# Optimization experiments

Measured on AMD Instinct MI355X. Metric: run time of the kernel, lower is better.

Reference implementation:

```python
import jax, jax.numpy as jnp
import numpy as np

SEQ = 4096
STATE_DIM = 512
ACTION_DIM = 496
T_DIM = 16
EMBED = STATE_DIM + ACTION_DIM + T_DIM  # 1024
HEADS = 4
HEAD_DIM = EMBED // HEADS
FF = 4096
N_EXP = 8
TOP_K = 2
EPS = 1e-5


def _ln(x, g, b):
    m = jnp.mean(x, -1, keepdims=True)
    v = jnp.var(x, -1, keepdims=True)
    return (x - m) * jax.lax.rsqrt(v + EPS) * g + b


def setup_inputs() -> dict:
    key = jax.random.key(0)
    ks = jax.random.split(key, 24)
    s = lambda k, shape, scale=0.02: jax.random.normal(k, shape, dtype=jnp.float32) * scale
    return {
        "x": jax.random.normal(ks[0], (SEQ, ACTION_DIM), dtype=jnp.float32),
        "time": jax.random.randint(ks[1], (SEQ,), 0, 6),
        "state": jax.random.normal(ks[2], (SEQ, 1, STATE_DIM), dtype=jnp.float32),
        "time_table": s(ks[3], (6, T_DIM), 1.0),
        "expert_w": s(ks[4], (N_EXP, EMBED, EMBED)),   # [n, in, out]
        "expert_b": jnp.zeros((N_EXP, EMBED), jnp.float32),
        "gate_w": s(ks[5], (EMBED, N_EXP)),
        "gate_b": jnp.zeros((N_EXP,), jnp.float32),
        "in_proj_w": s(ks[6], (EMBED, 3 * EMBED)),
        "in_proj_b": jnp.zeros((3 * EMBED,), jnp.float32),
        "out_proj_w": s(ks[7], (EMBED, EMBED)),
        "out_proj_b": jnp.zeros((EMBED,), jnp.float32),
        "ln1_g": jnp.ones((EMBED,), jnp.float32),
        "ln1_b": jnp.zeros((EMBED,), jnp.float32),
        "ff1_w": s(ks[8], (EMBED, FF)),
        "ff1_b": jnp.zeros((FF,), jnp.float32),
        "ff2_w": s(ks[9], (FF, ACTION_DIM)),
        "ff2_b": jnp.zeros((ACTION_DIM,), jnp.float32),
        "ln2_g": jnp.ones((ACTION_DIM,), jnp.float32),
        "ln2_b": jnp.zeros((ACTION_DIM,), jnp.float32),
    }


def reference(x, time, state, time_table, expert_w, expert_b, gate_w, gate_b,
              in_proj_w, in_proj_b, out_proj_w, out_proj_b,
              ln1_g, ln1_b, ff1_w, ff1_b, ff2_w, ff2_b, ln2_g, ln2_b):
    # combine inputs -> [S, EMBED]
    t_emb = time_table[time]                      # [S, t_dim]
    h = jnp.concatenate([x, t_emb, state[:, 0, :]], axis=-1)

    # MoE: softmax gate, top-k combine over densely-computed expert outputs
    gate = jax.nn.softmax(h @ gate_w + gate_b, axis=-1)      # [S, N]
    scores, idx = jax.lax.top_k(gate, TOP_K)                 # [S, K]
    all_out = jnp.einsum('se,nef->snf', h, expert_w) + expert_b[None]  # [S, N, E]
    comb = jnp.zeros_like(gate).at[jnp.arange(SEQ)[:, None], idx].add(scores)
    moe = jnp.einsum('sn,snf->sf', comb, all_out)            # [S, E]

    # multi-head self-attention (torch nn.MultiheadAttention, unbatched)
    qkv = moe @ in_proj_w + in_proj_b
    q, k, v = jnp.split(qkv, 3, axis=-1)
    q = q.reshape(SEQ, HEADS, HEAD_DIM) * (HEAD_DIM ** -0.5)
    k = k.reshape(SEQ, HEADS, HEAD_DIM)
    v = v.reshape(SEQ, HEADS, HEAD_DIM)
    att = jax.nn.softmax(jnp.einsum('shd,thd->hst', q, k), axis=-1)
    ao = jnp.einsum('hst,thd->shd', att, v).reshape(SEQ, EMBED)
    ao = ao @ out_proj_w + out_proj_b

    out1 = _ln(moe + ao, ln1_g, ln1_b)
    ff = jax.nn.relu(out1 @ ff1_w + ff1_b) @ ff2_w + ff2_b   # [S, action_dim]
    return _ln(ff, ln2_g, ln2_b)
```

## Files before the change

### kernel.cpp

```cpp
#include <hip/hip_runtime.h>
#include <hip/hip_bf16.h>
#include <hip/hip_fp8.h>

typedef __hip_bfloat16 hb;
typedef __bf16 bf16x8 __attribute__((ext_vector_type(8)));
typedef __bf16 bf16x4 __attribute__((ext_vector_type(4)));
typedef float f32x4 __attribute__((ext_vector_type(4)));

#define SEQ 4096
#define EMBED 1024
#define NHEAD 4
#define HDIM 256
#define FFD 4096
#define NEXP 8
#define ADIM 496
#define NSLOT 9216

static __device__ __forceinline__ float b2f(hb x) { return __bfloat162float(x); }
static __device__ __forceinline__ hb f2b(float x) { return __float2bfloat16(x); }
static __device__ __forceinline__ unsigned char f2e4m3(float v) {
  __hip_fp8_e4m3 t(v);
  return t.__x;
}
static __device__ __forceinline__ unsigned char f2e4m3_fast(float x) {
  unsigned u = __float_as_uint(x);
  u += 0x7FFFFu + ((u >> 20) & 1u);
  return (unsigned char)((u >> 20) - 960u);
}

#define GLOAD_LDS16(g, l)                                                      \
  __builtin_amdgcn_global_load_lds(                                            \
      (const __attribute__((address_space(1))) void*)(g),                      \
      (__attribute__((address_space(3))) void*)(l), 16, 0, 0)

#define GEMM_KLOOP64(KMAX)                                                     \
  for (int kt = 0; kt < (KMAX); kt += 64) {                                    \
    GLOAD_LDS16(Ag + kt, sA + wave * 512);                                     \
    GLOAD_LDS16(Ag + kt + 32, sA + 4096 + wave * 512);                         \
    GLOAD_LDS16(Ag + kt + 64 * lda_, sA + 2048 + wave * 512);                  \
    GLOAD_LDS16(Ag + kt + 64 * lda_ + 32, sA + 6144 + wave * 512);             \
    GLOAD_LDS16(Bg + kt, sB + wave * 512);                                     \
    GLOAD_LDS16(Bg + kt + 32, sB + 4096 + wave * 512);                         \
    GLOAD_LDS16(Bg + kt + 64 * ldb_, sB + 2048 + wave * 512);                  \
    GLOAD_LDS16(Bg + kt + 64 * ldb_ + 32, sB + 6144 + wave * 512);             \
    __syncthreads();                                                           \
    _Pragma("unroll") for (int ks = 0; ks < 2; ks++) {                         \
      bf16x8 av[4], bv[4];                                                     \
      _Pragma("unroll") for (int i = 0; i < 4; i++) {                          \
        const int row = wr * 64 + i * 16 + lm;                                 \
        av[i] = *(const bf16x8*)&sA[ks * 4096 + row * 32 + sw8];               \
      }                                                                        \
      _Pragma("unroll") for (int i = 0; i < 4; i++) {                          \
        const int row = wc * 64 + i * 16 + lm;                                 \
        bv[i] = *(const bf16x8*)&sB[ks * 4096 + row * 32 + sw8];               \
      }                                                                        \
      _Pragma("unroll") for (int i = 0; i < 4; i++)                            \
          _Pragma("unroll") for (int j = 0; j < 4; j++) acc[i][j] =            \
          __builtin_amdgcn_mfma_f32_16x16x32_bf16(av[i], bv[j], acc[i][j], 0,  \
                                                  0, 0);                       \
    }                                                                          \
    __syncthreads();                                                           \
  }

#define GEMM_PROLOGUE                                                          \
  const int m0 = blockIdx.y * 128, n0 = blockIdx.x * 128;                      \
  const int tid = threadIdx.x;                                                 \
  const int wave = tid >> 6, lane = tid & 63;                                  \
  const int quad = lane >> 4, lm = lane & 15;                                  \
  const int wr = wave >> 1, wc = wave & 1;                                     \
  const int r0 = tid >> 2;                                                     \
  const int cg = 8 * ((tid & 3) ^ ((tid >> 2) & 3));                           \
  const int sw8 = (quad ^ (lm & 3)) * 8;

#define EPILOGUE_B16(DST, LDC)                                                 \
  {                                                                            \
    hb* eb = smem + wave * 1024;                                               \
    _Pragma("unroll") for (int i = 0; i < 4; i++) {                            \
      _Pragma("unroll") for (int j = 0; j < 4; j++) {                          \
        const int c = ((j ^ quad) << 4) + lm;                                  \
        _Pragma("unroll") for (int rr = 0; rr < 4; rr++)                       \
            eb[(quad * 4 + rr) * 64 + c] = f2b(acc[i][j][rr]);                 \
      }                                                                        \
      _Pragma("unroll") for (int p = 0; p < 2; p++) {                          \
        const int r = p * 8 + (lane >> 3);                                     \
        const int cgc = lane & 7;                                              \
        const int gs = (cgc >> 1) ^ (r >> 2);                                  \
        const bf16x8 val =                                                     \
            *(const bf16x8*)&eb[r * 64 + gs * 16 + (cgc & 1) * 8];             \
        const long grow = m0 + wr * 64 + i * 16 + r;                           \
        *(bf16x8*)&DST[grow * (LDC) + n0 + wc * 64 + cgc * 8] = val;           \
      }                                                                        \
    }                                                                          \
  }

__global__ __launch_bounds__(256) void gemm_bt(
    const hb* __restrict__ A, long lda, long bA,
    const hb* __restrict__ B, long ldb, long bB,
    hb* __restrict__ C, long ldc, long bC,
    int K, const float* __restrict__ bias, int relu) {
  __shared__ __align__(16) hb smem[2 * 128 * 64];
  hb* sA = smem;
  hb* sB = smem + 8192;
  const int z = blockIdx.z;
  A += (long)z * bA;
  B += (long)z * bB;
  C += (long)z * bC;
  GEMM_PROLOGUE
  const long lda_ = lda, ldb_ = ldb;
  const hb* Ag = A + (long)(m0 + r0) * lda + cg;
  const hb* Bg = B + (long)(n0 + r0) * ldb + cg;

  f32x4 acc[4][4] = {};
  GEMM_KLOOP64(K)

  hb* eb = smem + wave * 1024;
#pragma unroll
  for (int i = 0; i < 4; i++) {
#pragma unroll
    for (int j = 0; j < 4; j++) {
      const float bval = bias ? bias[n0 + wc * 64 + j * 16 + lm] : 0.f;
      const int c = ((j ^ quad) << 4) + lm;
#pragma unroll
      for (int rr = 0; rr < 4; rr++) {
        float v = acc[i][j][rr] + bval;
        if (relu) v = fmaxf(v, 0.f);
        eb[(quad * 4 + rr) * 64 + c] = f2b(v);
      }
    }
#pragma unroll
    for (int p = 0; p < 2; p++) {
      const int r = p * 8 + (lane >> 3);
      const int cgc = lane & 7;
      const int gs = (cgc >> 1) ^ (r >> 2);
      const bf16x8 val = *(const bf16x8*)&eb[r * 64 + gs * 16 + (cgc & 1) * 8];
      const long grow = m0 + wr * 64 + i * 16 + r;
      *(bf16x8*)&C[grow * ldc + n0 + wc * 64 + cgc * 8] = val;
    }
  }
}

__global__ __launch_bounds__(256) void gemm_bt_exp(
    const hb* __restrict__ A, long lda, long bA,
    const hb* __restrict__ B, long ldb, long bB,
    unsigned char* __restrict__ C, long ldc, long bC,
    int K, float scale, hb* __restrict__ rsP) {
  __shared__ __align__(16) hb smem[2 * 128 * 64];
  hb* sA = smem;
  hb* sB = smem + 8192;
  const int z = blockIdx.z;
  A += (long)z * bA;
  B += (long)z * bB;
  C += (long)z * bC;
  GEMM_PROLOGUE
  const long lda_ = lda, ldb_ = ldb;
  const hb* Ag = A + (long)(m0 + r0) * lda + cg;
  const hb* Bg = B + (long)(n0 + r0) * ldb + cg;

  f32x4 acc[4][4] = {};
  GEMM_KLOOP64(K)

  unsigned char* eb8 = (unsigned char*)smem + wave * 1024;
  float* rbuf = (float*)sB;
  float rs[4][4];
#pragma unroll
  for (int i = 0; i < 4; i++) {
    float r4[4] = {0.f, 0.f, 0.f, 0.f};
#pragma unroll
    for (int j = 0; j < 4; j++) {
      const int c = ((j ^ quad) << 4) + lm;
#pragma unroll
      for (int rr = 0; rr < 4; rr++) {
        const float e =
            fminf(fmaxf(__expf(acc[i][j][rr] * scale), 0.015625f), 448.f);
        r4[rr] += e;
        eb8[(quad * 4 + rr) * 64 + c] = f2e4m3_fast(e);
      }
    }
#pragma unroll
    for (int rr = 0; rr < 4; rr++) {
      r4[rr] += __shfl_xor(r4[rr], 1);
      r4[rr] += __shfl_xor(r4[rr], 2);
      r4[rr] += __shfl_xor(r4[rr], 4);
      r4[rr] += __shfl_xor(r4[rr], 8);
      rs[i][rr] = r4[rr];
    }
    {
      const int r = lane >> 2;
      const int cgc = lane & 3;
      const f32x4 val =
          *(const f32x4*)&eb8[r * 64 + ((cgc ^ (r >> 2)) << 4)];
      const long grow = m0 + wr * 64 + i * 16 + r;
      *(f32x4*)&C[grow * ldc + n0 + wc * 64 + cgc * 16] = val;
    }
  }
  if (lm == 0) {
#pragma unroll
    for (int i = 0; i < 4; i++)
#pragma unroll
      for (int rr = 0; rr < 4; rr++)
        rbuf[(wr * 2 + wc) * 64 + i * 16 + quad * 4 + rr] = rs[i][rr];
  }
  __syncthreads();
  if (tid < 128) {
    const int lwr = tid >> 6, r64 = tid & 63;
    const float d = rbuf[lwr * 128 + r64] + rbuf[lwr * 128 + 64 + r64];
    rsP[((long)blockIdx.x * gridDim.z + z) * SEQ + m0 + lwr * 64 + r64] =
        f2b(d);
  }
}

__global__ __launch_bounds__(256) void pv_f8_splitk(
    const unsigned char* __restrict__ S, const unsigned char* __restrict__ Vt,
    hb* __restrict__ Cp) {
  const int z = blockIdx.z;
  const int head = z >> 1, split = z & 1;
  const unsigned char* A = S + (long)head * SEQ * SEQ + split * 2048;
  const unsigned char* B = Vt + ((long)head << 20) + split * 2048;
  hb* Cb = Cp + (long)z * SEQ * 256;
  __shared__ __align__(16) unsigned char smem8[16384];
  hb* smem = (hb*)smem8;
  unsigned char* sA8 = smem8;
  unsigned char* sB8 = smem8 + 8192;
  const int m0 = blockIdx.y * 128, n0 = blockIdx.x * 128;
  const int tid = threadIdx.x;
  const int wave = tid >> 6, lane = tid & 63;
  const int quad = lane >> 4, lm = lane & 15;
  const int wr = wave >> 1, wc = wave & 1;
  const int r8 = tid >> 2;
  const int cg8 = 16 * ((tid & 3) ^ (r8 & 3));
  const unsigned char* Ag = A + (long)(m0 + r8) * 4096 + cg8;
  const unsigned char* Bg = B + (long)(n0 + r8) * 4096 + cg8;

  f32x4 acc[4][4] = {};
  for (int kt = 0; kt < 2048; kt += 64) {
    GLOAD_LDS16(Ag + kt, sA8 + wave * 1024);
    GLOAD_LDS16(Ag + kt + 64 * 4096, sA8 + 4096 + wave * 1024);
    GLOAD_LDS16(Bg + kt, sB8 + wave * 1024);
    GLOAD_LDS16(Bg + kt + 64 * 4096, sB8 + 4096 + wave * 1024);
    __syncthreads();
#pragma unroll
    for (int ks = 0; ks < 2; ks++) {
      long a8[4], b8[4];
#pragma unroll
      for (int i = 0; i < 4; i++) {
        const int row = wr * 64 + i * 16 + lm;
        a8[i] = *(const long*)&sA8[row * 64 +
                                   (((ks * 2 + (quad >> 1)) ^ (row & 3)) << 4) +
                                   (quad & 1) * 8];
      }
#pragma unroll
      for (int i = 0; i < 4; i++) {
        const int row = wc * 64 + i * 16 + lm;
        b8[i] = *(const long*)&sB8[row * 64 +
                                   (((ks * 2 + (quad >> 1)) ^ (row & 3)) << 4) +
                                   (quad & 1) * 8];
      }
#pragma unroll
      for (int i = 0; i < 4; i++)
#pragma unroll
        for (int j = 0; j < 4; j++)
          acc[i][j] = __builtin_amdgcn_mfma_f32_16x16x32_fp8_fp8(
              a8[i], b8[j], acc[i][j], 0, 0, 0);
    }
    __syncthreads();
  }
  EPILOGUE_B16(Cb, 256)
}

__global__ __launch_bounds__(256) void gemm_bt_splitk(
    const hb* __restrict__ A, long lda, long bA,
    const hb* __restrict__ B, long ldb, long bB,
    float* __restrict__ Cp, int ldcp, long pstride, int Ksub, int shift) {
  const int z = blockIdx.z;
  const int batch = z >> shift, split = z - (batch << shift);
  A += (long)batch * bA + (long)split * Ksub;
  B += (long)batch * bB + (long)split * Ksub;
  Cp += (long)z * pstride;
  __shared__ __align__(16) hb smem[2 * 128 * 64];
  hb* sA = smem;
  hb* sB = smem + 8192;
  GEMM_PROLOGUE
  const long lda_ = lda, ldb_ = ldb;
  const hb* Ag = A + (long)(m0 + r0) * lda + cg;
  const hb* Bg = B + (long)(n0 + r0) * ldb + cg;

  f32x4 acc[4][4] = {};
  GEMM_KLOOP64(Ksub)

  float* ef = (float*)smem + wave * 1024;
#pragma unroll
  for (int i = 0; i < 4; i++) {
#pragma unroll
    for (int j = 0; j < 4; j++) {
      const int c = ((j ^ quad) << 4) + lm;
#pragma unroll
      for (int rr = 0; rr < 4; rr++)
        ef[(quad * 4 + rr) * 64 + c] = acc[i][j][rr];
    }
#pragma unroll
    for (int p = 0; p < 4; p++) {
      const int r = p * 4 + (lane >> 4);
      const int cgc = lane & 15;
      const int gs = (cgc >> 2) ^ (r >> 2);
      const f32x4 val = *(const f32x4*)&ef[r * 64 + gs * 16 + (cgc & 3) * 4];
      const long grow = m0 + wr * 64 + i * 16 + r;
      *(f32x4*)&Cp[grow * ldcp + n0 + wc * 64 + cgc * 4] = val;
    }
  }
}

__global__ __launch_bounds__(256) void gemm_bt_splitk_b16(
    const hb* __restrict__ A, long lda, long bA,
    const hb* __restrict__ B, long ldb, long bB,
    hb* __restrict__ Cp, int ldcp, long pstride, int Ksub, int shift) {
  const int z = blockIdx.z;
  const int batch = z >> shift, split = z - (batch << shift);
  A += (long)batch * bA + (long)split * Ksub;
  B += (long)batch * bB + (long)split * Ksub;
  Cp += (long)z * pstride;
  __shared__ __align__(16) hb smem[2 * 128 * 64];
  hb* sA = smem;
  hb* sB = smem + 8192;
  GEMM_PROLOGUE
  const long lda_ = lda, ldb_ = ldb;
  const hb* Ag = A + (long)(m0 + r0) * lda + cg;
  const hb* Bg = B + (long)(n0 + r0) * ldb + cg;

  f32x4 acc[4][4] = {};
  GEMM_KLOOP64(Ksub)
  EPILOGUE_B16(Cp, ldcp)
}

__global__ __launch_bounds__(256) void reduce_splitk(
    const float* __restrict__ part, long pstride, int nsplit, int shift,
    hb* __restrict__ C, long ldc, long bC, int Nshift) {
  const long idx = (long)blockIdx.x * 256 + threadIdx.x;
  const int batch = blockIdx.y;
  float v = 0.f;
  for (int k = 0; k < nsplit; k++)
    v += part[(long)((batch << shift) + k) * pstride + idx];
  const long row = idx >> Nshift;
  const long col = idx & ((1 << Nshift) - 1);
  C[(long)batch * bC + row * ldc + col] = f2b(v);
}

__global__ __launch_bounds__(256) void reduce_pv(
    const hb* __restrict__ part, const hb* __restrict__ rsP,
    hb* __restrict__ ao) {
  const int rb = blockIdx.x * 4, head = blockIdx.y, tid = threadIdx.x;
  __shared__ float dsh[4];
  if (tid < 128) {
    const int r = tid >> 5, nb = tid & 31;
    float p = b2f(rsP[((long)nb * NHEAD + head) * SEQ + rb + r]);
#pragma unroll
    for (int o = 16; o; o >>= 1) p += __shfl_down(p, o, 32);
    if (nb == 0) dsh[r] = p;
  }
  __syncthreads();
  const int r = tid >> 6, c4 = (tid & 63) * 4;
  const float den = dsh[r];
  const long base = ((long)(head * 2) * SEQ + rb + r) * 256 + c4;
  const bf16x4 p0 = *(const bf16x4*)&part[base];
  const bf16x4 p1 = *(const bf16x4*)&part[base + (long)SEQ * 256];
  bf16x4 o4;
#pragma unroll
  for (int k = 0; k < 4; k++)
    o4[k] = (__bf16)(((float)p0[k] + (float)p1[k]) / den);
  *(bf16x4*)&ao[(long)(rb + r) * 1024 + head * 256 + c4] = o4;
}

__global__ __launch_bounds__(256) void gemm_moe(
    const hb* __restrict__ h, const hb* __restrict__ expertT,
    const int* __restrict__ slot_token, const int* __restrict__ eblk,
    hb* __restrict__ slotout) {
  const int e = eblk[blockIdx.y];
  if (e < 0) return;
  __shared__ __align__(16) hb smem[2 * 128 * 64];
  hb* sA = smem;
  hb* sB = smem + 8192;
  GEMM_PROLOGUE
  const int t0 = slot_token[m0 + r0];
  const int t1 = slot_token[m0 + r0 + 64];
  const hb* B = expertT + ((long)e << 20);
  const hb* Ag0 = h + (long)t0 * EMBED + cg;
  const hb* Ag1 = h + (long)t1 * EMBED + cg;
  const hb* Bg = B + (long)(n0 + r0) * EMBED + cg;

  f32x4 acc[4][4] = {};
  for (int kt = 0; kt < EMBED; kt += 64) {
    GLOAD_LDS16(Ag0 + kt, sA + wave * 512);
    GLOAD_LDS16(Ag0 + kt + 32, sA + 4096 + wave * 512);
    GLOAD_LDS16(Ag1 + kt, sA + 2048 + wave * 512);
    GLOAD_LDS16(Ag1 + kt + 32, sA + 6144 + wave * 512);
    GLOAD_LDS16(Bg + kt, sB + wave * 512);
    GLOAD_LDS16(Bg + kt + 32, sB + 4096 + wave * 512);
    GLOAD_LDS16(Bg + kt + 64 * EMBED, sB + 2048 + wave * 512);
    GLOAD_LDS16(Bg + kt + 64 * EMBED + 32, sB + 6144 + wave * 512);
    __syncthreads();
#pragma unroll
    for (int ks = 0; ks < 2; ks++) {
      bf16x8 av[4], bv[4];
#pragma unroll
      for (int i = 0; i < 4; i++) {
        const int row = wr * 64 + i * 16 + lm;
        av[i] = *(const bf16x8*)&sA[ks * 4096 + row * 32 + sw8];
      }
#pragma unroll
      for (int i = 0; i < 4; i++) {
        const int row = wc * 64 + i * 16 + lm;
        bv[i] = *(const bf16x8*)&sB[ks * 4096 + row * 32 + sw8];
      }
#pragma unroll
      for (int i = 0; i < 4; i++)
#pragma unroll
        for (int j = 0; j < 4; j++)
          acc[i][j] = __builtin_amdgcn_mfma_f32_16x16x32_bf16(av[i], bv[j],
                                                              acc[i][j], 0, 0, 0);
    }
    __syncthreads();
  }
  EPILOGUE_B16(slotout, EMBED)
}

__global__ __launch_bounds__(256) void transpose_all(
    const float* __restrict__ expert_w, const float* __restrict__ in_proj_w,
    const float* __restrict__ out_proj_w, const float* __restrict__ ff1_w,
    const float* __restrict__ ff2_w, hb* __restrict__ expertT,
    hb* __restrict__ inprojT, hb* __restrict__ outprojT, hb* __restrict__ ff1T,
    hb* __restrict__ ff2T) {
  const int b = blockIdx.x;
  const float* in;
  hb* outp;
  int Cin, ldin, ldout, bx, by;
  if (b < 4096) {
    const int z = b >> 9, l = b & 511;
    bx = l & 31; by = l >> 5;
    in = expert_w + (long)z * 1048576; outp = expertT + (long)z * 1048576;
    Cin = 1024; ldin = 1024; ldout = 1024;
  } else if (b < 5632) {
    const int l = b - 4096;
    bx = l % 96; by = l / 96;
    in = in_proj_w; outp = inprojT;
    Cin = 3072; ldin = 3072; ldout = 1024;
  } else if (b < 6144) {
    const int l = b - 5632;
    bx = l & 31; by = l >> 5;
    in = out_proj_w; outp = outprojT;
    Cin = 1024; ldin = 1024; ldout = 1024;
  } else if (b < 8192) {
    const int l = b - 6144;
    bx = l & 127; by = l >> 7;
    in = ff1_w; outp = ff1T;
    Cin = 4096; ldin = 4096; ldout = 1024;
  } else {
    const int l = b - 8192;
    bx = l & 15; by = l >> 4;
    in = ff2_w; outp = ff2T;
    Cin = 496; ldin = 496; ldout = 4096;
  }
  __shared__ hb tile[32][72];
  const int c0 = bx * 32, r0 = by * 64;
  const int t = threadIdx.x;
  {
    const int rr = t >> 2, cb = (t & 3) * 8;
    const int c = c0 + cb;
    float v[8] = {0, 0, 0, 0, 0, 0, 0, 0};
    if (c < Cin) {
      const f32x4 p0 = *(const f32x4*)&in[(long)(r0 + rr) * ldin + c];
      const f32x4 p1 = *(const f32x4*)&in[(long)(r0 + rr) * ldin + c + 4];
#pragma unroll
      for (int k = 0; k < 4; k++) { v[k] = p0[k]; v[4 + k] = p1[k]; }
    }
#pragma unroll
    for (int j = 0; j < 8; j++) {
      const int cidx = cb + j;
      tile[cidx][rr ^ ((((cidx) >> 3) & 3) << 3)] = f2b(v[j]);
    }
  }
  __syncthreads();
  {
    const int oc = t >> 3, seg = t & 7;
    const bf16x8 val = *(const bf16x8*)&tile[oc][(seg ^ ((oc >> 3) & 3)) * 8];
    *(bf16x8*)&outp[(long)(c0 + oc) * ldout + r0 + seg * 8] = val;
  }
}

__global__ __launch_bounds__(256) void transpose_v(
    const hb* __restrict__ in, hb* __restrict__ out) {
  __shared__ hb tile[32][33];
  const int z = blockIdx.z;
  in += (long)z * 256;
  out += (long)z * 1048576;
  const int c0 = blockIdx.x * 32, r0 = blockIdx.y * 32;
  const int tx = threadIdx.x, ty = threadIdx.y;
#pragma unroll
  for (int i = 0; i < 32; i += 8)
    tile[ty + i][tx] = in[(long)(r0 + ty + i) * 3072 + c0 + tx];
  __syncthreads();
#pragma unroll
  for (int i = 0; i < 32; i += 8)
    out[(long)(c0 + ty + i) * 4096 + r0 + tx] = tile[tx][ty + i];
}

__global__ __launch_bounds__(256) void transpose_v8(
    const hb* __restrict__ in, unsigned char* __restrict__ out) {
  __shared__ hb tile[32][33];
  const int z = blockIdx.z;
  in += (long)z * 256;
  out += (long)z * 1048576;
  const int c0 = blockIdx.x * 32, r0 = blockIdx.y * 32;
  const int tx = threadIdx.x, ty = threadIdx.y;
#pragma unroll
  for (int i = 0; i < 32; i += 8)
    tile[ty + i][tx] = in[(long)(r0 + ty + i) * 3072 + c0 + tx];
  __syncthreads();
#pragma unroll
  for (int i = 0; i < 32; i += 8)
    out[(long)(c0 + ty + i) * 4096 + r0 + tx] = f2e4m3(b2f(tile[tx][ty + i]));
}

__global__ __launch_bounds__(256) void bh_gate_kernel(
    const float* __restrict__ x, const int* __restrict__ timev,
    const float* __restrict__ state, const float* __restrict__ ttab,
    const float* __restrict__ gw, const float* __restrict__ gb,
    hb* __restrict__ h, int* __restrict__ tok_e, float* __restrict__ tok_w) {
  const int s = blockIdx.x, tid = threadIdx.x;
  const int wv = tid >> 6, ln = tid & 63;
  const int t = timev[s];
  const int c = tid * 4;
  f32x4 v4;
  if (c < ADIM)
    v4 = *(const f32x4*)&x[(long)s * ADIM + c];
  else if (c < 512)
    v4 = *(const f32x4*)&ttab[t * 16 + (c - ADIM)];
  else
    v4 = *(const f32x4*)&state[(long)s * 512 + (c - 512)];
  bf16x4 h4;
#pragma unroll
  for (int k = 0; k < 4; k++) h4[k] = (__bf16)v4[k];
  *(bf16x4*)&h[(long)s * EMBED + c] = h4;
  float acc[8] = {0, 0, 0, 0, 0, 0, 0, 0};
#pragma unroll
  for (int k = 0; k < 4; k++) {
    const float* g = gw + (c + k) * 8;
#pragma unroll
    for (int n = 0; n < 8; n++) acc[n] += v4[k] * g[n];
  }
#pragma unroll
  for (int o = 32; o; o >>= 1)
#pragma unroll
    for (int n = 0; n < 8; n++) acc[n] += __shfl_down(acc[n], o);
  __shared__ float red[4][8];
  if (ln == 0)
#pragma unroll
    for (int n = 0; n < 8; n++) red[wv][n] = acc[n];
  __syncthreads();
  if (tid == 0) {
    float lg[8], m = -1e30f;
    for (int n = 0; n < 8; n++) {
      lg[n] = red[0][n] + red[1][n] + red[2][n] + red[3][n] + gb[n];
      m = fmaxf(m, lg[n]);
    }
    float den = 0.f;
    for (int n = 0; n < 8; n++) {
      lg[n] = expf(lg[n] - m);
      den += lg[n];
    }
    for (int n = 0; n < 8; n++) lg[n] /= den;
    int i1 = 0;
    for (int n = 1; n < 8; n++)
      if (lg[n] > lg[i1]) i1 = n;
    int i2 = (i1 == 0) ? 1 : 0;
    for (int n = 0; n < 8; n++) {
      if (n == i1) continue;
      if (lg[n] > lg[i2]) i2 = n;
    }
    tok_e[2 * s] = i1;
    tok_w[2 * s] = lg[i1];
    tok_e[2 * s + 1] = i2;
    tok_w[2 * s + 1] = lg[i2];
  }
}

__global__ __launch_bounds__(256) void group_kernel(
    const int* __restrict__ tok_e, int* __restrict__ slot_token,
    int* __restrict__ token_slot, int* __restrict__ eblk) {
  __shared__ int cnt[8], off[9], cur[8];
  const int tid = threadIdx.x;
  if (tid < 8) cnt[tid] = 0;
  for (int i = tid; i < NSLOT; i += 256) slot_token[i] = 0;
  __syncthreads();
  for (int i = tid; i < 2 * SEQ; i += 256) atomicAdd(&cnt[tok_e[i]], 1);
  __syncthreads();
  if (tid == 0) {
    int o = 0;
    for (int n = 0; n < 8; n++) {
      off[n] = o;
      cur[n] = o;
      o += (cnt[n] + 127) & ~127;
    }
    off[8] = o;
  }
  __syncthreads();
  if (tid < NSLOT / 128) {
    const int rb = tid * 128;
    int e = -1;
    for (int n = 0; n < 8; n++)
      if (rb >= off[n] && rb < off[n + 1]) e = n;
    eblk[tid] = e;
  }
  for (int i = tid; i < 2 * SEQ; i += 256) {
    const int e = tok_e[i];
    const int slot = atomicAdd(&cur[e], 1);
    slot_token[slot] = i >> 1;
    token_slot[i] = slot;
  }
}

__global__ __launch_bounds__(256) void moe_combine_kernel(
    const hb* __restrict__ slotout, const int* __restrict__ token_slot,
    const float* __restrict__ tok_w, const int* __restrict__ tok_e,
    const float* __restrict__ eb, hb* __restrict__ moe) {
  const int s = blockIdx.x, tid = threadIdx.x;
  const int s0 = token_slot[2 * s], s1 = token_slot[2 * s + 1];
  const float w0 = tok_w[2 * s], w1 = tok_w[2 * s + 1];
  const int e0 = tok_e[2 * s], e1 = tok_e[2 * s + 1];
  const int c = tid * 4;
  const bf16x4 a0 = *(const bf16x4*)&slotout[(long)s0 * EMBED + c];
  const bf16x4 a1 = *(const bf16x4*)&slotout[(long)s1 * EMBED + c];
  const f32x4 b0 = *(const f32x4*)&eb[e0 * EMBED + c];
  const f32x4 b1 = *(const f32x4*)&eb[e1 * EMBED + c];
  bf16x4 o4;
#pragma unroll
  for (int k = 0; k < 4; k++)
    o4[k] = (__bf16)(w0 * ((float)a0[k] + b0[k]) + w1 * ((float)a1[k] + b1[k]));
  *(bf16x4*)&moe[(long)s * EMBED + c] = o4;
}

__global__ __launch_bounds__(256) void softmax_fast(hb* __restrict__ S,
                                                    float scale) {
  const long row = blockIdx.x;
  const int tid = threadIdx.x, wv = tid >> 6, ln = tid & 63;
  hb* p = S + row * 4096 + tid * 16;
  __shared__ float red[4];
  bf16x8 a0 = *(const bf16x8*)p;
  bf16x8 a1 = *(const bf16x8*)(p + 8);
  float v[16];
#pragma unroll
  for (int i = 0; i < 8; i++) {
    v[i] = (float)a0[i];
    v[8 + i] = (float)a1[i];
  }
  float m = v[0];
#pragma unroll
  for (int i = 1; i < 16; i++) m = fmaxf(m, v[i]);
#pragma unroll
  for (int o = 32; o; o >>= 1) m = fmaxf(m, __shfl_down(m, o));
  if (ln == 0) red[wv] = m;
  __syncthreads();
  const float M = fmaxf(fmaxf(red[0], red[1]), fmaxf(red[2], red[3])) * scale;
  __syncthreads();
  float sum = 0.f;
#pragma unroll
  for (int i = 0; i < 16; i++) {
    v[i] = __expf(v[i] * scale - M);
    sum += v[i];
  }
#pragma unroll
  for (int o = 32; o; o >>= 1) sum += __shfl_down(sum, o);
  if (ln == 0) red[wv] = sum;
  __syncthreads();
  const float inv = 1.f / (red[0] + red[1] + red[2] + red[3]);
#pragma unroll
  for (int i = 0; i < 8; i++) {
    a0[i] = (__bf16)(v[i] * inv);
    a1[i] = (__bf16)(v[8 + i] * inv);
  }
  *(bf16x8*)p = a0;
  *(bf16x8*)(p + 8) = a1;
}

__global__ __launch_bounds__(256) void ln_kernel(
    const hb* __restrict__ in, long ldin, const hb* __restrict__ resid,
    long ldr, const float* __restrict__ g, const float* __restrict__ beta,
    hb* __restrict__ outb, long ldout, int ncol) {
  const int s = blockIdx.x, tid = threadIdx.x, wv = tid >> 6, ln = tid & 63;
  __shared__ float buf[1024];
  __shared__ float red[4];
  float sum = 0.f, sq = 0.f;
  for (int c = tid * 4; c < ncol; c += 1024) {
    const bf16x4 iv = *(const bf16x4*)&in[(long)s * ldin + c];
#pragma unroll
    for (int k = 0; k < 4; k++) {
      float v = (float)iv[k];
      buf[c + k] = v;
    }
    if (resid) {
      const bf16x4 rv = *(const bf16x4*)&resid[(long)s * ldr + c];
#pragma unroll
      for (int k = 0; k < 4; k++) buf[c + k] += (float)rv[k];
    }
#pragma unroll
    for (int k = 0; k < 4; k++) {
      const float v = buf[c + k];
      sum += v;
      sq += v * v;
    }
  }
#pragma unroll
  for (int o = 32; o; o >>= 1) sum += __shfl_down(sum, o);
  if (ln == 0) red[wv] = sum;
  __syncthreads();
  const float S = red[0] + red[1] + red[2] + red[3];
  __syncthreads();
#pragma unroll
  for (int o = 32; o; o >>= 1) sq += __shfl_down(sq, o);
  if (ln == 0) red[wv] = sq;
  __syncthreads();
  const float Q = red[0] + red[1] + red[2] + red[3];
  const float mean = S / ncol;
  const float var = Q / ncol - mean * mean;
  const float r = rsqrtf(var + 1e-5f);
  for (int c = tid * 4; c < ncol; c += 1024) {
    const f32x4 gv = *(const f32x4*)&g[c];
    const f32x4 bv = *(const f32x4*)&beta[c];
    bf16x4 o4;
#pragma unroll
    for (int k = 0; k < 4; k++)
      o4[k] = (__bf16)((buf[c + k] - mean) * r * gv[k] + bv[k]);
    *(bf16x4*)&outb[(long)s * ldout + c] = o4;
  }
}

__global__ __launch_bounds__(256) void ln2_red_kernel(
    const float* __restrict__ part, long pstride,
    const float* __restrict__ bias, const float* __restrict__ g,
    const float* __restrict__ beta, float* __restrict__ out) {
  const int s = blockIdx.x, tid = threadIdx.x, wv = tid >> 6, ln = tid & 63;
  __shared__ float buf[512];
  __shared__ float red[4];
  float sum = 0.f, sq = 0.f;
  for (int c = tid; c < ADIM; c += 256) {
    const long idx = (long)s * 512 + c;
    float v = part[idx] + part[pstride + idx] + part[2 * pstride + idx] +
              part[3 * pstride + idx] + bias[c];
    buf[c] = v;
    sum += v;
    sq += v * v;
  }
#pragma unroll
  for (int o = 32; o; o >>= 1) sum += __shfl_down(sum, o);
  if (ln == 0) red[wv] = sum;
  __syncthreads();
  const float S = red[0] + red[1] + red[2] + red[3];
  __syncthreads();
#pragma unroll
  for (int o = 32; o; o >>= 1) sq += __shfl_down(sq, o);
  if (ln == 0) red[wv] = sq;
  __syncthreads();
  const float Q = red[0] + red[1] + red[2] + red[3];
  const float mean = S / ADIM;
  const float var = Q / ADIM - mean * mean;
  const float r = rsqrtf(var + 1e-5f);
  for (int c = tid; c < ADIM; c += 256)
    out[(long)s * ADIM + c] = (buf[c] - mean) * r * g[c] + beta[c];
}

__global__ __launch_bounds__(256) void ln2_red_b16_kernel(
    const hb* __restrict__ part, long pstride,
    const float* __restrict__ bias, const float* __restrict__ g,
    const float* __restrict__ beta, float* __restrict__ out) {
  const int s = blockIdx.x, tid = threadIdx.x, wv = tid >> 6, ln = tid & 63;
  __shared__ float buf[512];
  __shared__ float red[4];
  float sum = 0.f, sq = 0.f;
  const int c = tid * 4;
  if (c < ADIM) {
    const long idx = (long)s * 512 + c;
    const bf16x4 p0 = *(const bf16x4*)&part[idx];
    const bf16x4 p1 = *(const bf16x4*)&part[pstride + idx];
    const bf16x4 p2 = *(const bf16x4*)&part[2 * pstride + idx];
    const bf16x4 p3 = *(const bf16x4*)&part[3 * pstride + idx];
    const f32x4 bv = *(const f32x4*)&bias[c];
#pragma unroll
    for (int k = 0; k < 4; k++) {
      const float v = (float)p0[k] + (float)p1[k] + (float)p2[k] +
                      (float)p3[k] + bv[k];
      buf[c + k] = v;
      sum += v;
      sq += v * v;
    }
  }
#pragma unroll
  for (int o = 32; o; o >>= 1) sum += __shfl_down(sum, o);
  if (ln == 0) red[wv] = sum;
  __syncthreads();
  const float S = red[0] + red[1] + red[2] + red[3];
  __syncthreads();
#pragma unroll
  for (int o = 32; o; o >>= 1) sq += __shfl_down(sq, o);
  if (ln == 0) red[wv] = sq;
  __syncthreads();
  const float Q = red[0] + red[1] + red[2] + red[3];
  const float mean = S / ADIM;
  const float var = Q / ADIM - mean * mean;
  const float r = rsqrtf(var + 1e-5f);
  if (c < ADIM) {
    const f32x4 gv = *(const f32x4*)&g[c];
    const f32x4 bt = *(const f32x4*)&beta[c];
    f32x4 o4;
#pragma unroll
    for (int k = 0; k < 4; k++)
      o4[k] = (buf[c + k] - mean) * r * gv[k] + bt[k];
    *(f32x4*)&out[(long)s * ADIM + c] = o4;
  }
}

extern "C" void kernel_launch(void* const* d_in, const int* in_sizes, int n_in,
                              void* d_out, int out_size, void* d_ws,
                              size_t ws_size, hipStream_t stream) {
  const float* x = (const float*)d_in[0];
  const int* timev = (const int*)d_in[1];
  const float* state = (const float*)d_in[2];
  const float* ttab = (const float*)d_in[3];
  const float* expert_w = (const float*)d_in[4];
  const float* expert_b = (const float*)d_in[5];
  const float* gate_w = (const float*)d_in[6];
  const float* gate_b = (const float*)d_in[7];
  const float* in_proj_w = (const float*)d_in[8];
  const float* in_proj_b = (const float*)d_in[9];
  const float* out_proj_w = (const float*)d_in[10];
  const float* out_proj_b = (const float*)d_in[11];
  const float* ln1_g = (const float*)d_in[12];
  const float* ln1_b = (const float*)d_in[13];
  const float* ff1_w = (const float*)d_in[14];
  const float* ff1_b = (const float*)d_in[15];
  const float* ff2_w = (const float*)d_in[16];
  const float* ff2_b = (const float*)d_in[17];
  const float* ln2_g = (const float*)d_in[18];
  const float* ln2_b = (const float*)d_in[19];
  float* out = (float*)d_out;

  char* w = (char*)d_ws;
  const long MB = 1048576;
  const bool big = ws_size >= (size_t)(192 * MB);

  hb* expertT = (hb*)(w + 0 * MB);
  hb* slotout = (hb*)(w + 16 * MB);
  hb* h = (hb*)(w + 35 * MB);
  hb* inprojT = (hb*)(w + 43 * MB);
  hb* outprojT = (hb*)(w + (big ? 168 : 49) * MB);
  hb* ff1T = (hb*)(w + (big ? 170 : 51) * MB);
  hb* ff2T = (hb*)(w + (big ? 178 : 59) * MB);
  const long metaOff = (big ? 190 : 63) * MB;
  int* tok_e = (int*)(w + metaOff);
  float* tok_w = (float*)(w + metaOff + 32768);
  int* slot_token = (int*)(w + metaOff + 65536);
  int* token_slot = (int*)(w + metaOff + 102400);
  int* eblk = (int*)(w + metaOff + 135168);
  hb* rsP = (hb*)(w + metaOff + 163840);
  hb* moe = (hb*)(w + (big ? 152 : 64) * MB);
  hb* qkv = (hb*)(w + (big ? 0 : 72) * MB);
  unsigned char* scores8 = (unsigned char*)(w + 24 * MB);
  hb* scores = (hb*)(w + 96 * MB);
  unsigned char* vt8 = (unsigned char*)(w + 160 * MB);
  hb* vt = (hb*)(w + 8 * MB);
  hb* ao = (hb*)(w + (big ? 182 : 0) * MB);
  hb* ao2 = (hb*)(w + (big ? 24 : 8) * MB);
  hb* out1 = (hb*)(w + (big ? 32 : 132) * MB);
  hb* ffmid = (hb*)(w + (big ? 40 : 96) * MB);
  float* part = (float*)(w + (big ? 72 : 16) * MB);
  hb* partb16 = (hb*)(w + (big ? 72 : 16) * MB);
  hb* pvpart = (hb*)(w + 0 * MB);
  (void)in_sizes; (void)n_in; (void)out_size;

  transpose_all<<<dim3(9216), dim3(256), 0, stream>>>(
      expert_w, in_proj_w, out_proj_w, ff1_w, ff2_w, expertT, inprojT, outprojT,
      ff1T, ff2T);

  bh_gate_kernel<<<dim3(SEQ), 256, 0, stream>>>(x, timev, state, ttab, gate_w,
                                                gate_b, h, tok_e, tok_w);
  group_kernel<<<dim3(1), 256, 0, stream>>>(tok_e, slot_token, token_slot, eblk);

  gemm_moe<<<dim3(8, NSLOT / 128), 256, 0, stream>>>(h, expertT, slot_token,
                                                     eblk, slotout);
  moe_combine_kernel<<<dim3(SEQ), 256, 0, stream>>>(slotout, token_slot, tok_w,
                                                    tok_e, expert_b, moe);

  gemm_bt<<<dim3(24, 32, 1), 256, 0, stream>>>(moe, 1024, 0, inprojT, 1024, 0,
                                               qkv, 3072, 0, 1024, in_proj_b, 0);
  if (big)
    transpose_v8<<<dim3(8, 128, 4), dim3(32, 8), 0, stream>>>(qkv + 2048, vt8);
  else
    transpose_v<<<dim3(8, 128, 4), dim3(32, 8), 0, stream>>>(qkv + 2048, vt);

  if (big) {
    gemm_bt_exp<<<dim3(32, 32, 4), 256, 0, stream>>>(
        qkv, 3072, 256, qkv + 1024, 3072, 256, scores8, 4096, (long)SEQ * SEQ,
        HDIM, 0.0625f, rsP);
    pv_f8_splitk<<<dim3(2, 32, 8), 256, 0, stream>>>(scores8, vt8, pvpart);
    reduce_pv<<<dim3(1024, 4), 256, 0, stream>>>(pvpart, rsP, ao);
  } else {
    for (int hp = 0; hp < 2; ++hp) {
      const hb* qb = qkv + hp * 512;
      const hb* kb = qkv + 1024 + hp * 512;
      gemm_bt<<<dim3(32, 32, 2), 256, 0, stream>>>(
          qb, 3072, 256, kb, 3072, 256, scores, 4096, (long)SEQ * SEQ, HDIM,
          nullptr, 0);
      softmax_fast<<<dim3(2 * SEQ), 256, 0, stream>>>(scores, 0.0625f);
      gemm_bt_splitk<<<dim3(2, 32, 8), 256, 0, stream>>>(
          scores, 4096, (long)SEQ * SEQ, vt + (long)hp * 2097152, 4096,
          1048576L, part, 256, (long)SEQ * 256, 1024, 2);
      reduce_splitk<<<dim3(4096, 2), 256, 0, stream>>>(
          part, (long)SEQ * 256, 4, 2, ao + hp * 512, 1024, 256, 8);
    }
  }

  gemm_bt<<<dim3(8, 32, 1), 256, 0, stream>>>(ao, 1024, 0, outprojT, 1024, 0,
                                              ao2, 1024, 0, 1024, out_proj_b, 0);
  ln_kernel<<<dim3(SEQ), 256, 0, stream>>>(moe, 1024, ao2, 1024, ln1_g, ln1_b,
                                           out1, 1024, 1024);

  gemm_bt<<<dim3(32, 32, 1), 256, 0, stream>>>(out1, 1024, 0, ff1T, 1024, 0,
                                               ffmid, 4096, 0, 1024, ff1_b, 1);
  if (big) {
    gemm_bt_splitk_b16<<<dim3(4, 32, 4), 256, 0, stream>>>(
        ffmid, 4096, 0, ff2T, 4096, 0, partb16, 512, (long)SEQ * 512, 1024, 2);
    ln2_red_b16_kernel<<<dim3(SEQ), 256, 0, stream>>>(
        partb16, (long)SEQ * 512, ff2_b, ln2_g, ln2_b, out);
  } else {
    gemm_bt_splitk<<<dim3(4, 32, 4), 256, 0, stream>>>(
        ffmid, 4096, 0, ff2T, 4096, 0, part, 512, (long)SEQ * 512, 1024, 2);
    ln2_red_kernel<<<dim3(SEQ), 256, 0, stream>>>(part, (long)SEQ * 512, ff2_b,
                                                  ln2_g, ln2_b, out);
  }
}
```

Measured before the change: 514.7 us.

## Emit Q/K as fp8 from QKV GEMM and compute attention scores with fp8 MFMA

The QKV projection epilogue now writes Q and K columns directly as e4m3 fp8 into a separate buffer, while V stays bf16. The QK^T score kernel is replaced by an fp8×fp8 MFMA kernel that reads these fp8 operands, halving operand bytes and using the faster fp8 matrix instructions. This trades away Q/K precision: the attention logits are computed from fp8-quantized inputs, which adds error.

Result: no change. 512.2 us (-0.5%).

```diff
diff --git a/kernel.cpp b/kernel.cpp
--- a/kernel.cpp
+++ b/kernel.cpp
@@ -139,28 +139,110 @@
   }
 }
 
-__global__ __launch_bounds__(256) void gemm_bt_exp(
-    const hb* __restrict__ A, long lda, long bA,
-    const hb* __restrict__ B, long ldb, long bB,
-    unsigned char* __restrict__ C, long ldc, long bC,
-    int K, float scale, hb* __restrict__ rsP) {
+__global__ __launch_bounds__(256) void gemm_bt_qkv(
+    const hb* __restrict__ A, const hb* __restrict__ B,
+    hb* __restrict__ C, const float* __restrict__ bias,
+    unsigned char* __restrict__ qk8) {
   __shared__ __align__(16) hb smem[2 * 128 * 64];
   hb* sA = smem;
   hb* sB = smem + 8192;
+  GEMM_PROLOGUE
+  const long lda_ = 1024, ldb_ = 1024;
+  const hb* Ag = A + (long)(m0 + r0) * 1024 + cg;
+  const hb* Bg = B + (long)(n0 + r0) * 1024 + cg;
+
+  f32x4 acc[4][4] = {};
+  GEMM_KLOOP64(1024)
+
+  hb* eb = smem + wave * 1024;
+  const bool doq = (n0 < 2048);
+#pragma unroll
+  for (int i = 0; i < 4; i++) {
+#pragma unroll
+    for (int j = 0; j < 4; j++) {
+      const float bval = bias[n0 + wc * 64 + j * 16 + lm];
+      const int c = ((j ^ quad) << 4) + lm;
+#pragma unroll
+      for (int rr = 0; rr < 4; rr++)
+        eb[(quad * 4 + rr) * 64 + c] = f2b(acc[i][j][rr] + bval);
+    }
+#pragma unroll
+    for (int p = 0; p < 2; p++) {
+      const int r = p * 8 + (lane >> 3);
+      const int cgc = lane & 7;
+      const int gs = (cgc >> 1) ^ (r >> 2);
+      const bf16x8 val = *(const bf16x8*)&eb[r * 64 + gs * 16 + (cgc & 1) * 8];
+      const long grow = m0 + wr * 64 + i * 16 + r;
+      const int col = n0 + wc * 64 + cgc * 8;
+      if (doq) {
+        unsigned long long p8 = 0;
+#pragma unroll
+        for (int k = 0; k < 8; k++)
+          p8 |= (unsigned long long)f2e4m3((float)val[k]) << (8 * k);
+        *(unsigned long long*)&qk8[grow * 2048 + col] = p8;
+      } else {
+        *(bf16x8*)&C[grow * 3072 + col] = val;
+      }
+    }
+  }
+}
+
+__global__ __launch_bounds__(256) void qk_exp_f8(
+    const unsigned char* __restrict__ qk8, unsigned char* __restrict__ C,
+    float scale, hb* __restrict__ rsP) {
   const int z = blockIdx.z;
-  A += (long)z * bA;
-  B += (long)z * bB;
-  C += (long)z * bC;
-  GEMM_PROLOGUE
-  const long lda_ = lda, ldb_ = ldb;
-  const hb* Ag = A + (long)(m0 + r0) * lda + cg;
-  const hb* Bg = B + (long)(n0 + r0) * ldb + cg;
+  const unsigned char* A = qk8 + z * 256;
+  const unsigned char* B = qk8 + 1024 + z * 256;
+  unsigned char* Cb = C + (long)z * SEQ * SEQ;
+  __shared__ __align__(16) unsigned char smem8[16384];
+  unsigned char* sA8 = smem8;
+  unsigned char* sB8 = smem8 + 8192;
+  const int m0 = blockIdx.y * 128, n0 = blockIdx.x * 128;
+  const int tid = threadIdx.x;
+  const int wave = tid >> 6, lane = tid & 63;
+  const int quad = lane >> 4, lm = lane & 15;
+  const int wr = wave >> 1, wc = wave & 1;
+  const int r8 = tid >> 2;
+  const int cg8 = 16 * ((tid & 3) ^ (r8 & 3));
+  const unsigned char* Ag = A + (long)(m0 + r8) * 2048 + cg8;
+  const unsigned char* Bg = B + (long)(n0 + r8) * 2048 + cg8;
 
   f32x4 acc[4][4] = {};
-  GEMM_KLOOP64(K)
-
-  unsigned char* eb8 = (unsigned char*)smem + wave * 1024;
-  float* rbuf = (float*)sB;
+  for (int kt = 0; kt < 256; kt += 64) {
+    GLOAD_LDS16(Ag + kt, sA8 + wave * 1024);
+    GLOAD_LDS16(Ag + kt + 64 * 2048, sA8 + 4096 + wave * 1024);
+    GLOAD_LDS16(Bg + kt, sB8 + wave * 1024);
+    GLOAD_LDS16(Bg + kt + 64 * 2048, sB8 + 4096 + wave * 1024);
+    __syncthreads();
+#pragma unroll
+    for (int ks = 0; ks < 2; ks++) {
+      long a8[4], b8[4];
+#pragma unroll
+      for (int i = 0; i < 4; i++) {
+        const int row = wr * 64 + i * 16 + lm;
+        a8[i] = *(const long*)&sA8[row * 64 +
+                                   (((ks * 2 + (quad >> 1)) ^ (row & 3)) << 4) +
+                                   (quad & 1) * 8];
+      }
+#pragma unroll
+      for (int i = 0; i < 4; i++) {
+        const int row = wc * 64 + i * 16 + lm;
+        b8[i] = *(const long*)&sB8[row * 64 +
+                                   (((ks * 2 + (quad >> 1)) ^ (row & 3)) << 4) +
+                                   (quad & 1) * 8];
+      }
+#pragma unroll
+      for (int i = 0; i < 4; i++)
+#pragma unroll
+        for (int j = 0; j < 4; j++)
+          acc[i][j] = __builtin_amdgcn_mfma_f32_16x16x32_fp8_fp8(
+              a8[i], b8[j], acc[i][j], 0, 0, 0);
+    }
+    __syncthreads();
+  }
+
+  unsigned char* eb8 = smem8 + wave * 1024;
+  float* rbuf = (float*)(smem8 + 8192);
   float rs[4][4];
 #pragma unroll
   for (int i = 0; i < 4; i++) {
@@ -190,7 +272,7 @@
       const f32x4 val =
           *(const f32x4*)&eb8[r * 64 + ((cgc ^ (r >> 2)) << 4)];
       const long grow = m0 + wr * 64 + i * 16 + r;
-      *(f32x4*)&C[grow * ldc + n0 + wc * 64 + cgc * 16] = val;
+      *(f32x4*)&Cb[grow * 4096 + n0 + wc * 64 + cgc * 16] = val;
     }
   }
   if (lm == 0) {
@@ -204,8 +286,7 @@
   if (tid < 128) {
     const int lwr = tid >> 6, r64 = tid & 63;
     const float d = rbuf[lwr * 128 + r64] + rbuf[lwr * 128 + 64 + r64];
-    rsP[((long)blockIdx.x * gridDim.z + z) * SEQ + m0 + lwr * 64 + r64] =
-        f2b(d);
+    rsP[((long)blockIdx.x * NHEAD + z) * SEQ + m0 + lwr * 64 + r64] = f2b(d);
   }
 }
 
@@ -863,6 +944,7 @@
   hb* qkv = (hb*)(w + (big ? 0 : 72) * MB);
   unsigned char* scores8 = (unsigned char*)(w + 24 * MB);
   hb* scores = (hb*)(w + 96 * MB);
+  unsigned char* qk8 = (unsigned char*)(w + 88 * MB);
   unsigned char* vt8 = (unsigned char*)(w + 160 * MB);
   hb* vt = (hb*)(w + 8 * MB);
   hb* ao = (hb*)(w + (big ? 182 : 0) * MB);
@@ -887,17 +969,19 @@
   moe_combine_kernel<<<dim3(SEQ), 256, 0, stream>>>(slotout, token_slot, tok_w,
                                                     tok_e, expert_b, moe);
 
-  gemm_bt<<<dim3(24, 32, 1), 256, 0, stream>>>(moe, 1024, 0, inprojT, 1024, 0,
-                                               qkv, 3072, 0, 1024, in_proj_b, 0);
-  if (big)
+  if (big) {
+    gemm_bt_qkv<<<dim3(24, 32), 256, 0, stream>>>(moe, inprojT, qkv,
+                                                  in_proj_b, qk8);
     transpose_v8<<<dim3(8, 128, 4), dim3(32, 8), 0, stream>>>(qkv + 2048, vt8);
-  else
+  } else {
+    gemm_bt<<<dim3(24, 32, 1), 256, 0, stream>>>(moe, 1024, 0, inprojT, 1024,
+                                                 0, qkv, 3072, 0, 1024,
+                                                 in_proj_b, 0);
     transpose_v<<<dim3(8, 128, 4), dim3(32, 8), 0, stream>>>(qkv + 2048, vt);
+  }
 
   if (big) {
-    gemm_bt_exp<<<dim3(32, 32, 4), 256, 0, stream>>>(
-        qkv, 3072, 256, qkv + 1024, 3072, 256, scores8, 4096, (long)SEQ * SEQ,
-        HDIM, 0.0625f, rsP);
+    qk_exp_f8<<<dim3(32, 32, 4), 256, 0, stream>>>(qk8, scores8, 0.0625f, rsP);
     pv_f8_splitk<<<dim3(2, 32, 8), 256, 0, stream>>>(scores8, vt8, pvpart);
     reduce_pv<<<dim3(1024, 4), 256, 0, stream>>>(pvpart, rsP, ao);
   } else {
```
